# Kernel optimization log

Hardware: AMD Instinct MI355X
Metric: run time of the kernel (lower is better)

The kernel has to match this reference:

```python
import jax, jax.numpy as jnp
import numpy as np

N = 100000
E = 1600000
NFEAT, NHID, NCLASS = 500, 128, 40


def setup_inputs() -> dict:
    key = jax.random.key(0)
    ks = jax.random.split(key, 12)
    x = jax.random.normal(ks[0], (N, NFEAT), dtype=jnp.float32)
    row = jax.random.randint(ks[1], (E,), 0, N, dtype=jnp.int32)
    col = jax.random.randint(ks[2], (E,), 0, N, dtype=jnp.int32)
    # precomputed normalized adjacency values (D^-1/2 A D^-1/2 style)
    edge_weight = jax.random.uniform(ks[3], (E,), dtype=jnp.float32) / 16.0
    def lin(k, fi, fo):
        s = 1.0 / np.sqrt(fi)
        return jax.random.uniform(k, (fi, fo), dtype=jnp.float32, minval=-s, maxval=s)
    return {
        "x": x, "row": row, "col": col, "edge_weight": edge_weight,
        "W1": lin(ks[4], NFEAT, NHID), "b1": jnp.zeros((NHID,), jnp.float32),
        "W2": lin(ks[5], NHID, NHID), "b2": jnp.zeros((NHID,), jnp.float32),
        "W3": lin(ks[6], NHID, NHID), "b3": jnp.zeros((NHID,), jnp.float32),
        "W4": lin(ks[7], NHID, NCLASS), "b4": jnp.zeros((NCLASS,), jnp.float32),
    }


def gcn_layer(h, row, col, edge_weight, W, b):
    # support = h @ W ; out = spmm(adj, support) + b  (Kipf GraphConvolution)
    support = h @ W                                   # [N, Fout]
    msgs = edge_weight[:, None] * support[col]        # [E, Fout] gather on source nodes
    agg = jax.ops.segment_sum(msgs, row, num_segments=N)  # scatter-add to dest nodes
    return agg + b


def reference(x, row, col, edge_weight, W1, b1, W2, b2, W3, b3, W4, b4):
    # dropout is identity in eval mode (training=False)
    h = jax.nn.relu(gcn_layer(x, row, col, edge_weight, W1, b1))
    h = jax.nn.relu(gcn_layer(h, row, col, edge_weight, W2, b2))
    h = jax.nn.relu(gcn_layer(h, row, col, edge_weight, W3, b3))
    h = gcn_layer(h, row, col, edge_weight, W4, b4)
    return jax.nn.log_softmax(h, axis=1)
```

## Files before the change

### kernel.cpp

```cpp
#include <hip/hip_runtime.h>
#include <cstdint>
#include <cstddef>

#define NFEAT 500
#define NHID  128
#define NCLASS 40

typedef __attribute__((ext_vector_type(8))) short bf16x8;
typedef __attribute__((ext_vector_type(4))) float f32x4;

__device__ __forceinline__ unsigned short f2bf(float f) {
    union { float f; unsigned u; } v; v.f = f;
    unsigned u = v.u;
    unsigned r = u + 0x7FFF + ((u >> 16) & 1);
    return (unsigned short)(r >> 16);
}
__device__ __forceinline__ float bf2f(unsigned short h) {
    union { unsigned u; float f; } v; v.u = ((unsigned)h) << 16; return v.f;
}


__global__ void k_hist(const int* __restrict__ row, int E, int* __restrict__ counts) {
    int i = blockIdx.x * 256 + threadIdx.x;
    if (i < E) atomicAdd(&counts[row[i]], 1);
}

__global__ void k_block_sum(const int* __restrict__ counts, int n, int* __restrict__ partials) {
    __shared__ int tmp[256];
    int i = blockIdx.x * 256 + threadIdx.x;
    tmp[threadIdx.x] = (i < n) ? counts[i] : 0;
    __syncthreads();
    for (int o = 128; o > 0; o >>= 1) {
        if (threadIdx.x < o) tmp[threadIdx.x] += tmp[threadIdx.x + o];
        __syncthreads();
    }
    if (threadIdx.x == 0) partials[blockIdx.x] = tmp[0];
}

__global__ void k_scan_partials(int* __restrict__ partials, int nb) {
    __shared__ int tmp[512];
    int t = threadIdx.x;
    int v = (t < nb) ? partials[t] : 0;
    tmp[t] = v;
    __syncthreads();
    for (int o = 1; o < 512; o <<= 1) {
        int add = (t >= o) ? tmp[t - o] : 0;
        __syncthreads();
        tmp[t] += add;
        __syncthreads();
    }
    if (t < nb) partials[t] = tmp[t] - v;
}

__global__ void k_scan_counts(int* __restrict__ counts, const int* __restrict__ partials,
                              int* __restrict__ row_ptr, int n) {
    __shared__ int tmp[256];
    int t = threadIdx.x;
    int i = blockIdx.x * 256 + t;
    int v = (i < n) ? counts[i] : 0;
    tmp[t] = v;
    __syncthreads();
    for (int o = 1; o < 256; o <<= 1) {
        int add = (t >= o) ? tmp[t - o] : 0;
        __syncthreads();
        tmp[t] += add;
        __syncthreads();
    }
    int incl = tmp[t];
    int base = partials[blockIdx.x];
    if (i < n) {
        row_ptr[i] = base + incl - v;
        counts[i] = 0;
    }
    if (i == n - 1) row_ptr[n] = base + incl;
}

__global__ void k_scatter(const int* __restrict__ row, const int* __restrict__ col,
                          const float* __restrict__ w, int E,
                          const int* __restrict__ row_ptr, int* __restrict__ cursor,
                          uint2* __restrict__ csr_cw) {
    int i = blockIdx.x * 256 + threadIdx.x;
    if (i < E) {
        int r = row[i];
        int p = row_ptr[r] + atomicAdd(&cursor[r], 1);
        csr_cw[p] = make_uint2((unsigned)col[i], __float_as_uint(w[i]));
    }
}


__global__ void k_prep_w(const float* __restrict__ W, unsigned short* __restrict__ Wt,
                         int K, int Norig, int Nt, int Kpad) {
    int idx = blockIdx.x * 256 + threadIdx.x;
    if (idx >= Nt * Kpad) return;
    int n = idx / Kpad, k = idx % Kpad;
    unsigned short v = 0;
    if (k < K && n < Norig) v = f2bf(W[(size_t)k * Norig + n]);
    Wt[idx] = v;
}


template<bool AFP32, int KPAD, int BN, int CN, int CPITCH>
__global__ __launch_bounds__(256) void k_gemm_direct(const void* __restrict__ Ain,
                                                     const unsigned short* __restrict__ Wt,
                                                     unsigned short* __restrict__ C,
                                                     int M, int K) {
    constexpr int TM = 2;
    constexpr int TN = BN / 16;
    constexpr int NIT = KPAD / 32;
    const int t = threadIdx.x;
    const int lane = t & 63;
    const int w = t >> 6;
    const int l15 = lane & 15, quad = lane >> 4;
    const int rbase = blockIdx.x * 128 + w * 32;

    const float* Af = (const float*)Ain;
    const unsigned short* Ab = (const unsigned short*)Ain;

    f32x4 acc[TM][TN];
#pragma unroll
    for (int mi = 0; mi < TM; mi++)
#pragma unroll
        for (int ni = 0; ni < TN; ni++)
            acc[mi][ni] = (f32x4){0.f, 0.f, 0.f, 0.f};

    int rowi[TM];
#pragma unroll
    for (int mi = 0; mi < TM; mi++) {
        int r = rbase + mi * 16 + l15;
        rowi[mi] = AFP32 ? min(r, M - 1) : r;
    }

    float4 fA[2][TM][2];
    bf16x8 hA[2][TM];
    bf16x8 hB[2][TN];

    auto loadA = [&](int set, int k0) {
        if (AFP32) {
            int gk = k0 + quad * 8;
#pragma unroll
            for (int mi = 0; mi < TM; mi++) {
                const float* p = Af + (size_t)rowi[mi] * K + gk;
                fA[set][mi][0] = (gk + 4 <= K) ? *(const float4*)p : make_float4(0.f, 0.f, 0.f, 0.f);
                fA[set][mi][1] = (gk + 8 <= K) ? *(const float4*)(p + 4) : make_float4(0.f, 0.f, 0.f, 0.f);
            }
        } else {
#pragma unroll
            for (int mi = 0; mi < TM; mi++)
                hA[set][mi] = *(const bf16x8*)(Ab + (size_t)rowi[mi] * KPAD + k0 + quad * 8);
        }
    };
    auto loadB = [&](int set, int k0) {
#pragma unroll
        for (int ni = 0; ni < TN; ni++)
            hB[set][ni] = *(const bf16x8*)(Wt + (size_t)(ni * 16 + l15) * KPAD + k0 + quad * 8);
    };
    auto compute = [&](int set) {
        bf16x8 afr[TM];
#pragma unroll
        for (int mi = 0; mi < TM; mi++) {
            if (AFP32) {
                float4 u = fA[set][mi][0], v = fA[set][mi][1];
                bf16x8 r;
                r[0] = (short)f2bf(u.x); r[1] = (short)f2bf(u.y);
                r[2] = (short)f2bf(u.z); r[3] = (short)f2bf(u.w);
                r[4] = (short)f2bf(v.x); r[5] = (short)f2bf(v.y);
                r[6] = (short)f2bf(v.z); r[7] = (short)f2bf(v.w);
                afr[mi] = r;
            } else {
                afr[mi] = hA[set][mi];
            }
        }
#pragma unroll
        for (int mi = 0; mi < TM; mi++)
#pragma unroll
            for (int ni = 0; ni < TN; ni++)
                acc[mi][ni] = __builtin_amdgcn_mfma_f32_16x16x32_bf16(afr[mi], hB[set][ni], acc[mi][ni], 0, 0, 0);
    };

    loadA(0, 0);
    loadB(0, 0);
    for (int it = 0; it < NIT; it += 2) {
        if (it + 1 < NIT) { loadA(1, (it + 1) * 32); loadB(1, (it + 1) * 32); }
        compute(0);
        if (it + 2 < NIT) { loadA(0, (it + 2) * 32); loadB(0, (it + 2) * 32); }
        if (it + 1 < NIT) compute(1);
    }

#pragma unroll
    for (int mi = 0; mi < TM; mi++) {
#pragma unroll
        for (int r = 0; r < 4; r++) {
            int gm = rbase + mi * 16 + quad * 4 + r;
#pragma unroll
            for (int ni = 0; ni < TN; ni++) {
                int gn = ni * 16 + l15;
                if (gn < CN) C[(size_t)gm * CPITCH + gn] = f2bf(acc[mi][ni][r]);
            }
        }
    }
}


__global__ __launch_bounds__(256) void k_spmm128(const unsigned short* __restrict__ S,
                                                 const int* __restrict__ rp,
                                                 const uint2* __restrict__ cw,
                                                 const float* __restrict__ bias,
                                                 unsigned short* __restrict__ out,
                                                 int n, int do_relu) {
    int wid  = threadIdx.x >> 6;
    int lane = threadIdx.x & 63;
    int node = blockIdx.x * 4 + wid;
    if (node >= n) return;
    int s = rp[node], e = rp[node + 1];
    float a0x = 0.f, a0y = 0.f, a1x = 0.f, a1y = 0.f;
    float a2x = 0.f, a2y = 0.f, a3x = 0.f, a3y = 0.f;
    int i = s;
    for (; i + 4 <= e; i += 4) {
        uint2 e0 = cw[i], e1 = cw[i + 1], e2 = cw[i + 2], e3 = cw[i + 3];
        unsigned v0 = ((const unsigned*)(S + (size_t)e0.x * NHID))[lane];
        unsigned v1 = ((const unsigned*)(S + (size_t)e1.x * NHID))[lane];
        unsigned v2 = ((const unsigned*)(S + (size_t)e2.x * NHID))[lane];
        unsigned v3 = ((const unsigned*)(S + (size_t)e3.x * NHID))[lane];
        float w0 = __uint_as_float(e0.y), w1 = __uint_as_float(e1.y);
        float w2 = __uint_as_float(e2.y), w3 = __uint_as_float(e3.y);
        a0x = fmaf(w0, bf2f((unsigned short)v0), a0x); a0y = fmaf(w0, bf2f((unsigned short)(v0 >> 16)), a0y);
        a1x = fmaf(w1, bf2f((unsigned short)v1), a1x); a1y = fmaf(w1, bf2f((unsigned short)(v1 >> 16)), a1y);
        a2x = fmaf(w2, bf2f((unsigned short)v2), a2x); a2y = fmaf(w2, bf2f((unsigned short)(v2 >> 16)), a2y);
        a3x = fmaf(w3, bf2f((unsigned short)v3), a3x); a3y = fmaf(w3, bf2f((unsigned short)(v3 >> 16)), a3y);
    }
    for (; i < e; i++) {
        uint2 e0 = cw[i];
        unsigned v0 = ((const unsigned*)(S + (size_t)e0.x * NHID))[lane];
        float w0 = __uint_as_float(e0.y);
        a0x = fmaf(w0, bf2f((unsigned short)v0), a0x); a0y = fmaf(w0, bf2f((unsigned short)(v0 >> 16)), a0y);
    }
    float ax = (a0x + a1x) + (a2x + a3x) + bias[lane * 2];
    float ay = (a0y + a1y) + (a2y + a3y) + bias[lane * 2 + 1];
    if (do_relu) {
        ax = fmaxf(ax, 0.f);
        ay = fmaxf(ay, 0.f);
    }
    unsigned o = (unsigned)f2bf(ax) | ((unsigned)f2bf(ay) << 16);
    __builtin_nontemporal_store(o, (unsigned*)(out + (size_t)node * NHID) + lane);
}


__global__ __launch_bounds__(256) void k_spmm40_lsm(const unsigned short* __restrict__ S,
                                                    const int* __restrict__ rp,
                                                    const uint2* __restrict__ cw,
                                                    const float* __restrict__ bias,
                                                    float* __restrict__ out,
                                                    int n) {
    int wid  = threadIdx.x >> 6;
    int lane = threadIdx.x & 63;
    int node = blockIdx.x * 4 + wid;
    if (node >= n) return;
    int s = rp[node], e = rp[node + 1];
    float a0 = 0.f, a1 = 0.f, a2 = 0.f, a3 = 0.f;
    int i = s;
    bool act = lane < NCLASS;
    for (; i + 4 <= e; i += 4) {
        uint2 e0 = cw[i], e1 = cw[i + 1], e2 = cw[i + 2], e3 = cw[i + 3];
        if (act) {
            float v0 = bf2f(S[(size_t)e0.x * NCLASS + lane]);
            float v1 = bf2f(S[(size_t)e1.x * NCLASS + lane]);
            float v2 = bf2f(S[(size_t)e2.x * NCLASS + lane]);
            float v3 = bf2f(S[(size_t)e3.x * NCLASS + lane]);
            a0 = fmaf(__uint_as_float(e0.y), v0, a0);
            a1 = fmaf(__uint_as_float(e1.y), v1, a1);
            a2 = fmaf(__uint_as_float(e2.y), v2, a2);
            a3 = fmaf(__uint_as_float(e3.y), v3, a3);
        }
    }
    for (; i < e; i++) {
        uint2 e0 = cw[i];
        if (act) a0 = fmaf(__uint_as_float(e0.y), bf2f(S[(size_t)e0.x * NCLASS + lane]), a0);
    }
    float acc = (a0 + a1) + (a2 + a3);
    float logit = act ? acc + bias[lane] : -INFINITY;
    float m = logit;
#pragma unroll
    for (int o = 32; o >= 1; o >>= 1) m = fmaxf(m, __shfl_xor(m, o, 64));
    float ex = act ? expf(logit - m) : 0.f;
    float ssum = ex;
#pragma unroll
    for (int o = 32; o >= 1; o >>= 1) ssum += __shfl_xor(ssum, o, 64);
    if (act) {
        float r = logit - m - logf(ssum);
        __builtin_nontemporal_store(r, out + (size_t)node * NCLASS + lane);
    }
}


extern "C" void kernel_launch(void* const* d_in, const int* in_sizes, int n_in,
                              void* d_out, int out_size, void* d_ws, size_t ws_size,
                              hipStream_t stream) {
    const float* x  = (const float*)d_in[0];
    const int* row  = (const int*)d_in[1];
    const int* col  = (const int*)d_in[2];
    const float* ew = (const float*)d_in[3];
    const float* W1 = (const float*)d_in[4];
    const float* b1 = (const float*)d_in[5];
    const float* W2 = (const float*)d_in[6];
    const float* b2 = (const float*)d_in[7];
    const float* W3 = (const float*)d_in[8];
    const float* b3 = (const float*)d_in[9];
    const float* W4 = (const float*)d_in[10];
    const float* b4 = (const float*)d_in[11];
    float* out = (float*)d_out;

    const int Nn = in_sizes[0] / NFEAT;
    const int E  = in_sizes[1];
    const int NB = (Nn + 255) / 256;
    const int Mpad = (Nn + 127) & ~127;

    char* ws = (char*)d_ws;
    size_t off = 0;
    auto alloc = [&](size_t bytes) {
        size_t o = off;
        off = (off + bytes + 255) & ~(size_t)255;
        return o;
    };
    int*   row_ptr  = (int*)(ws + alloc((size_t)(Nn + 1) * 4));
    int*   counts   = (int*)(ws + alloc((size_t)Nn * 4));
    int*   partials = (int*)(ws + alloc((size_t)NB * 4));
    uint2* csr_cw   = (uint2*)(ws + alloc((size_t)E * 8));
    unsigned short* Sb  = (unsigned short*)(ws + alloc((size_t)Mpad * NHID * 2));
    unsigned short* Hb  = (unsigned short*)(ws + alloc((size_t)Mpad * NHID * 2));
    unsigned short* S4b = (unsigned short*)(ws + alloc((size_t)Mpad * NCLASS * 2));
    unsigned short* Wt1 = (unsigned short*)(ws + alloc((size_t)128 * 512 * 2));
    unsigned short* Wt2 = (unsigned short*)(ws + alloc((size_t)128 * 128 * 2));
    unsigned short* Wt3 = (unsigned short*)(ws + alloc((size_t)128 * 128 * 2));
    unsigned short* Wt4 = (unsigned short*)(ws + alloc((size_t)48 * 128 * 2));

    k_prep_w<<<(128 * 512 + 255) / 256, 256, 0, stream>>>(W1, Wt1, NFEAT, NHID, 128, 512);
    k_prep_w<<<(128 * 128 + 255) / 256, 256, 0, stream>>>(W2, Wt2, NHID, NHID, 128, 128);
    k_prep_w<<<(128 * 128 + 255) / 256, 256, 0, stream>>>(W3, Wt3, NHID, NHID, 128, 128);
    k_prep_w<<<(48 * 128 + 255) / 256, 256, 0, stream>>>(W4, Wt4, NHID, NCLASS, 48, 128);

    (void)hipMemsetAsync(counts, 0, (size_t)Nn * 4, stream);
    k_hist<<<(E + 255) / 256, 256, 0, stream>>>(row, E, counts);
    k_block_sum<<<NB, 256, 0, stream>>>(counts, Nn, partials);
    k_scan_partials<<<1, 512, 0, stream>>>(partials, NB);
    k_scan_counts<<<NB, 256, 0, stream>>>(counts, partials, row_ptr, Nn);
    k_scatter<<<(E + 255) / 256, 256, 0, stream>>>(row, col, ew, E, row_ptr, counts, csr_cw);

    const int gblocks = Mpad / 128;
    const int spmm_blocks = (Nn + 3) / 4;

    k_gemm_direct<true, 512, 128, 128, 128><<<gblocks, 256, 0, stream>>>(x, Wt1, Sb, Nn, NFEAT);
    k_spmm128<<<spmm_blocks, 256, 0, stream>>>(Sb, row_ptr, csr_cw, b1, Hb, Nn, 1);
    k_gemm_direct<false, 128, 128, 128, 128><<<gblocks, 256, 0, stream>>>(Hb, Wt2, Sb, Nn, NHID);
    k_spmm128<<<spmm_blocks, 256, 0, stream>>>(Sb, row_ptr, csr_cw, b2, Hb, Nn, 1);
    k_gemm_direct<false, 128, 128, 128, 128><<<gblocks, 256, 0, stream>>>(Hb, Wt3, Sb, Nn, NHID);
    k_spmm128<<<spmm_blocks, 256, 0, stream>>>(Sb, row_ptr, csr_cw, b3, Hb, Nn, 1);
    k_gemm_direct<false, 128, 48, 40, 40><<<gblocks, 256, 0, stream>>>(Hb, Wt4, S4b, Nn, NHID);
    k_spmm40_lsm<<<spmm_blocks, 256, 0, stream>>>(S4b, row_ptr, csr_cw, b4, out, Nn);
}
```

Before: 893.2 us.

## Stage GEMM A tiles into LDS via async global_load_lds double buffering

Replaces per-lane register loads of the A operand in the dense GEMMs with global_load_lds transfers into a double-buffered shared-memory tile. Each block then reads MFMA fragments from LDS. The goal is fully coalesced row-contiguous global reads and overlap of the next tile's fetch with the current MFMA work. In exchange it adds a __syncthreads per K step and LDS pressure, and the fp32 path clamps columns near K rather than zero-padding them.

```diff
diff --git a/kernel.cpp b/kernel.cpp
--- a/kernel.cpp
+++ b/kernel.cpp
@@ -100,18 +100,21 @@
 
 
 template<bool AFP32, int KPAD, int BN, int CN, int CPITCH>
-__global__ __launch_bounds__(256) void k_gemm_direct(const void* __restrict__ Ain,
-                                                     const unsigned short* __restrict__ Wt,
-                                                     unsigned short* __restrict__ C,
-                                                     int M, int K) {
+__global__ __launch_bounds__(256) void k_gemm_lds(const void* __restrict__ Ain,
+                                                  const unsigned short* __restrict__ Wt,
+                                                  unsigned short* __restrict__ C,
+                                                  int M, int K) {
     constexpr int TM = 2;
     constexpr int TN = BN / 16;
+    constexpr int TB = AFP32 ? 16384 : 8192;
     constexpr int NIT = KPAD / 32;
+    __shared__ unsigned char As[2][TB];
+
     const int t = threadIdx.x;
     const int lane = t & 63;
     const int w = t >> 6;
     const int l15 = lane & 15, quad = lane >> 4;
-    const int rbase = blockIdx.x * 128 + w * 32;
+    const int mbase = blockIdx.x * 128;
 
     const float* Af = (const float*)Ain;
     const unsigned short* Ab = (const unsigned short*)Ain;
@@ -123,43 +126,53 @@
         for (int ni = 0; ni < TN; ni++)
             acc[mi][ni] = (f32x4){0.f, 0.f, 0.f, 0.f};
 
-    int rowi[TM];
-#pragma unroll
-    for (int mi = 0; mi < TM; mi++) {
-        int r = rbase + mi * 16 + l15;
-        rowi[mi] = AFP32 ? min(r, M - 1) : r;
-    }
-
-    float4 fA[2][TM][2];
-    bf16x8 hA[2][TM];
     bf16x8 hB[2][TN];
-
-    auto loadA = [&](int set, int k0) {
+    auto loadB = [&](int s, int k0) {
+#pragma unroll
+        for (int ni = 0; ni < TN; ni++)
+            hB[s][ni] = *(const bf16x8*)(Wt + (size_t)(ni * 16 + l15) * KPAD + k0 + quad * 8);
+    };
+
+    auto stage = [&](int b, int k0) {
+        unsigned char* lb = &As[b][0];
         if (AFP32) {
-            int gk = k0 + quad * 8;
-#pragma unroll
-            for (int mi = 0; mi < TM; mi++) {
-                const float* p = Af + (size_t)rowi[mi] * K + gk;
-                fA[set][mi][0] = (gk + 4 <= K) ? *(const float4*)p : make_float4(0.f, 0.f, 0.f, 0.f);
-                fA[set][mi][1] = (gk + 8 <= K) ? *(const float4*)(p + 4) : make_float4(0.f, 0.f, 0.f, 0.f);
+            int m_ = t >> 1, half = t & 1;
+            int grow = mbase + m_; grow = grow < M ? grow : M - 1;
+#pragma unroll
+            for (int p = 0; p < 4; p++) {
+                int col = k0 + p * 8 + half * 4;
+                col = (col + 4 <= K) ? col : K - 4;
+                const float* g = Af + (size_t)grow * K + col;
+                __builtin_amdgcn_global_load_lds(
+                    (const __attribute__((address_space(1))) void*)g,
+                    (__attribute__((address_space(3))) void*)(lb + p * 4096 + w * 1024 + lane * 16),
+                    16, 0, 0);
             }
         } else {
-#pragma unroll
-            for (int mi = 0; mi < TM; mi++)
-                hA[set][mi] = *(const bf16x8*)(Ab + (size_t)rowi[mi] * KPAD + k0 + quad * 8);
+            int m_ = t & 127;
+            int kcl = t >> 7;
+#pragma unroll
+            for (int p = 0; p < 2; p++) {
+                int kc = p * 2 + kcl;
+                const unsigned short* g = Ab + (size_t)(mbase + m_) * KPAD + k0 + kc * 8;
+                __builtin_amdgcn_global_load_lds(
+                    (const __attribute__((address_space(1))) void*)g,
+                    (__attribute__((address_space(3))) void*)(lb + p * 4096 + w * 1024 + lane * 16),
+                    16, 0, 0);
+            }
         }
     };
-    auto loadB = [&](int set, int k0) {
-#pragma unroll
-        for (int ni = 0; ni < TN; ni++)
-            hB[set][ni] = *(const bf16x8*)(Wt + (size_t)(ni * 16 + l15) * KPAD + k0 + quad * 8);
-    };
-    auto compute = [&](int set) {
+
+    auto compute = [&](int b, int s) {
+        const unsigned char* lb = &As[b][0];
         bf16x8 afr[TM];
 #pragma unroll
         for (int mi = 0; mi < TM; mi++) {
+            int m = w * 32 + mi * 16 + l15;
             if (AFP32) {
-                float4 u = fA[set][mi][0], v = fA[set][mi][1];
+                size_t off = ((size_t)quad * 128 + m) * 32;
+                float4 u = *(const float4*)(lb + off);
+                float4 v = *(const float4*)(lb + off + 16);
                 bf16x8 r;
                 r[0] = (short)f2bf(u.x); r[1] = (short)f2bf(u.y);
                 r[2] = (short)f2bf(u.z); r[3] = (short)f2bf(u.w);
@@ -167,30 +180,37 @@
                 r[6] = (short)f2bf(v.z); r[7] = (short)f2bf(v.w);
                 afr[mi] = r;
             } else {
-                afr[mi] = hA[set][mi];
+                size_t off = ((size_t)quad * 128 + m) * 16;
+                afr[mi] = *(const bf16x8*)(lb + off);
             }
         }
 #pragma unroll
         for (int mi = 0; mi < TM; mi++)
 #pragma unroll
             for (int ni = 0; ni < TN; ni++)
-                acc[mi][ni] = __builtin_amdgcn_mfma_f32_16x16x32_bf16(afr[mi], hB[set][ni], acc[mi][ni], 0, 0, 0);
+                acc[mi][ni] = __builtin_amdgcn_mfma_f32_16x16x32_bf16(afr[mi], hB[s][ni], acc[mi][ni], 0, 0, 0);
     };
 
-    loadA(0, 0);
     loadB(0, 0);
-    for (int it = 0; it < NIT; it += 2) {
-        if (it + 1 < NIT) { loadA(1, (it + 1) * 32); loadB(1, (it + 1) * 32); }
-        compute(0);
-        if (it + 2 < NIT) { loadA(0, (it + 2) * 32); loadB(0, (it + 2) * 32); }
-        if (it + 1 < NIT) compute(1);
+    stage(0, 0);
+    __syncthreads();
+
+    for (int it = 0; it < NIT; it++) {
+        const int cur = it & 1;
+        const bool more = (it + 1) < NIT;
+        if (more) {
+            loadB(cur ^ 1, (it + 1) * 32);
+            stage(cur ^ 1, (it + 1) * 32);
+        }
+        compute(cur, cur);
+        if (more) __syncthreads();
     }
 
 #pragma unroll
     for (int mi = 0; mi < TM; mi++) {
 #pragma unroll
         for (int r = 0; r < 4; r++) {
-            int gm = rbase + mi * 16 + quad * 4 + r;
+            int gm = mbase + w * 32 + mi * 16 + quad * 4 + r;
 #pragma unroll
             for (int ni = 0; ni < TN; ni++) {
                 int gn = ni * 16 + l15;
@@ -348,12 +368,12 @@
     const int gblocks = Mpad / 128;
     const int spmm_blocks = (Nn + 3) / 4;
 
-    k_gemm_direct<true, 512, 128, 128, 128><<<gblocks, 256, 0, stream>>>(x, Wt1, Sb, Nn, NFEAT);
+    k_gemm_lds<true, 512, 128, 128, 128><<<gblocks, 256, 0, stream>>>(x, Wt1, Sb, Nn, NFEAT);
     k_spmm128<<<spmm_blocks, 256, 0, stream>>>(Sb, row_ptr, csr_cw, b1, Hb, Nn, 1);
-    k_gemm_direct<false, 128, 128, 128, 128><<<gblocks, 256, 0, stream>>>(Hb, Wt2, Sb, Nn, NHID);
+    k_gemm_lds<false, 128, 128, 128, 128><<<gblocks, 256, 0, stream>>>(Hb, Wt2, Sb, Nn, NHID);
     k_spmm128<<<spmm_blocks, 256, 0, stream>>>(Sb, row_ptr, csr_cw, b2, Hb, Nn, 1);
-    k_gemm_direct<false, 128, 128, 128, 128><<<gblocks, 256, 0, stream>>>(Hb, Wt3, Sb, Nn, NHID);
+    k_gemm_lds<false, 128, 128, 128, 128><<<gblocks, 256, 0, stream>>>(Hb, Wt3, Sb, Nn, NHID);
     k_spmm128<<<spmm_blocks, 256, 0, stream>>>(Sb, row_ptr, csr_cw, b3, Hb, Nn, 1);
-    k_gemm_direct<false, 128, 48, 40, 40><<<gblocks, 256, 0, stream>>>(Hb, Wt4, S4b, Nn, NHID);
+    k_gemm_lds<false, 128, 48, 40, 40><<<gblocks, 256, 0, stream>>>(Hb, Wt4, S4b, Nn, NHID);
     k_spmm40_lsm<<<spmm_blocks, 256, 0, stream>>>(S4b, row_ptr, csr_cw, b4, out, Nn);
 }
```

Result: no change. 879.6 us (-1.5%).
